# Optimization experiments

Hardware: AMD Instinct MI355X
Metric: run time of the kernel (lower is better)

The kernel has to match this reference:

```python
import jax, jax.numpy as jnp
import numpy as np

D_MODEL = 1024
D_STATE = 16
D_CONV = 4
EXPAND = 2
NUM_LAYERS = 2
SEQ = 1024
BATCH = 2
D_INNER = EXPAND * D_MODEL          # 2048
DT_RANK = (D_MODEL + 15) // 16      # 64 (math.ceil(d_model/16))


def setup_inputs() -> dict:
    key = jax.random.key(0)
    ks = jax.random.split(key, 10)
    s = 0.02
    # A initialized as in mamba_ssm: A = repeat(arange(1, d_state+1), d_inner) -> A_log = log(A)
    A_log = jnp.log(jnp.broadcast_to(
        jnp.arange(1, D_STATE + 1, dtype=jnp.float32), (NUM_LAYERS, D_INNER, D_STATE)))
    return {
        "pe": jax.random.normal(ks[0], (SEQ, D_MODEL), jnp.float32) * s,
        "condition": jax.random.normal(ks[1], (BATCH, SEQ, D_MODEL), jnp.float32),
        "W_in": jax.random.normal(ks[2], (NUM_LAYERS, 2 * D_INNER, D_MODEL), jnp.float32) * s,
        "conv_w": jax.random.normal(ks[3], (NUM_LAYERS, D_INNER, D_CONV), jnp.float32) * s,
        "conv_b": jnp.zeros((NUM_LAYERS, D_INNER), jnp.float32),
        "W_x": jax.random.normal(ks[4], (NUM_LAYERS, DT_RANK + 2 * D_STATE, D_INNER), jnp.float32) * s,
        "W_dt": jax.random.normal(ks[5], (NUM_LAYERS, D_INNER, DT_RANK), jnp.float32) * s,
        "b_dt": jax.random.normal(ks[6], (NUM_LAYERS, D_INNER), jnp.float32) * s,
        "A_log": A_log,
        "Dp": jnp.ones((NUM_LAYERS, D_INNER), jnp.float32),
        "W_out": jax.random.normal(ks[7], (NUM_LAYERS, D_MODEL, D_INNER), jnp.float32) * s,
        "output_shape": BATCH,
    }


def _mamba_block(x, W_in, conv_w, conv_b, W_x, W_dt, b_dt, A_log, Dp, W_out):
    # x: [B, L, d_model]
    B, L, _ = x.shape
    xz = jnp.einsum('bld,ed->ble', x, W_in)          # [B, L, 2*d_inner]
    u, z = jnp.split(xz, 2, axis=-1)                 # each [B, L, d_inner]
    # causal depthwise conv1d (padding=d_conv-1, truncate to L)
    xp = jnp.pad(u, ((0, 0), (D_CONV - 1, 0), (0, 0)))
    xc = conv_b + sum(conv_w[:, k] * xp[:, k:k + L, :] for k in range(D_CONV))
    xc = jax.nn.silu(xc)                             # [B, L, d_inner]
    x_dbl = jnp.einsum('bld,ed->ble', xc, W_x)       # [B, L, dt_rank + 2*d_state]
    dt, Bm, Cm = jnp.split(x_dbl, [DT_RANK, DT_RANK + D_STATE], axis=-1)
    delta = jax.nn.softplus(jnp.einsum('blr,dr->bld', dt, W_dt) + b_dt)  # [B, L, d_inner]
    A = -jnp.exp(A_log)                              # [d_inner, d_state]

    def step(h, inputs):
        u_t, d_t, B_t, C_t = inputs                  # [B,di],[B,di],[B,ds],[B,ds]
        dA = jnp.exp(d_t[:, :, None] * A)            # [B, di, ds]
        h = dA * h + (d_t * u_t)[:, :, None] * B_t[:, None, :]
        y = jnp.einsum('bds,bs->bd', h, C_t)
        return h, y

    h0 = jnp.zeros((B, D_INNER, D_STATE), x.dtype)
    xs = (xc.transpose(1, 0, 2), delta.transpose(1, 0, 2),
          Bm.transpose(1, 0, 2), Cm.transpose(1, 0, 2))
    _, ys = jax.lax.scan(step, h0, xs)               # ys: [L, B, d_inner]
    y = ys.transpose(1, 0, 2) + xc * Dp
    out = y * jax.nn.silu(z)
    return jnp.einsum('bld,ed->ble', out, W_out)     # [B, L, d_model]


def reference(pe, condition, W_in, conv_w, conv_b, W_x, W_dt, b_dt, A_log, Dp, W_out, output_shape):
    # pe.repeat(B,1,1) + condition
    x = pe[None, :, :] + condition
    for i in range(NUM_LAYERS):
        x = _mamba_block(x, W_in[i], conv_w[i], conv_b[i], W_x[i],
                         W_dt[i], b_dt[i], A_log[i], Dp[i], W_out[i])
    return x
```

## Files before the change

### kernel.cpp

```cpp
#include <hip/hip_runtime.h>
#include <math.h>

#define D_MODEL 1024
#define D_INNER 2048
#define D_STATE 16
#define DT_RANK 64
#define SEQ 1024
#define BATCH 2
#define NLAYERS 2
#define ROWS (BATCH*SEQ)
#define XDIM 96
#define XZLD (2*D_INNER)

#define NC 32
#define CL 32
#define SDB 256

#define G2_ROWS 64
#define G2_KC 128
#define G2_BK 32
#define G2_KS (D_INNER / G2_KC)

typedef short bf16x8 __attribute__((ext_vector_type(8)));
typedef float f32x4  __attribute__((ext_vector_type(4)));

__device__ __forceinline__ unsigned short f2bf(float f) {
    union { float f; unsigned int u; } v; v.f = f;
    unsigned int u = v.u;
    return (unsigned short)((u + 0x7FFFu + ((u >> 16) & 1u)) >> 16);
}
__device__ __forceinline__ float bf2f(unsigned short u) {
    union { unsigned int i; float f; } v; v.i = ((unsigned int)u) << 16; return v.f;
}

__device__ __forceinline__ void gload_lds16(const void* g, void* s) {
    __builtin_amdgcn_global_load_lds((const __attribute__((address_space(1))) void*)g,
                                     (__attribute__((address_space(3))) void*)s, 16, 0, 0);
}

__global__ __launch_bounds__(256) void add_pe_kernel(const float* __restrict__ pe,
    const float* __restrict__ cond, float* __restrict__ X)
{
    int i = blockIdx.x * 256 + threadIdx.x;
    int total = ROWS * D_MODEL / 4;
    if (i >= total) return;
    int row  = i / (D_MODEL / 4);
    int l    = row & (SEQ - 1);
    int col4 = i - row * (D_MODEL / 4);
    float4 p = reinterpret_cast<const float4*>(pe)[l * (D_MODEL / 4) + col4];
    float4 c = reinterpret_cast<const float4*>(cond)[i];
    float4 r; r.x = p.x + c.x; r.y = p.y + c.y; r.z = p.z + c.z; r.w = p.w + c.w;
    reinterpret_cast<float4*>(X)[i] = r;
}

__global__ __launch_bounds__(256) void conv_bf16_dense(const float* __restrict__ src,
    unsigned short* __restrict__ dst, int n4)
{
    int i = blockIdx.x * 256 + threadIdx.x;
    if (i >= n4) return;
    float4 v = reinterpret_cast<const float4*>(src)[i];
    ushort4 o; o.x = f2bf(v.x); o.y = f2bf(v.y); o.z = f2bf(v.z); o.w = f2bf(v.w);
    reinterpret_cast<ushort4*>(dst)[i] = o;
}

#define WN1 (NLAYERS * 2 * D_INNER * D_MODEL / 4)
#define WN2 (NLAYERS * D_MODEL * D_INNER / 4)
#define WN3 (NLAYERS * D_INNER * DT_RANK / 4)
#define WN4 (ROWS * D_MODEL / 4)
__global__ __launch_bounds__(256) void conv_wall(const float* __restrict__ Win,
    const float* __restrict__ Wout, const float* __restrict__ Wdt,
    const float* __restrict__ pe, const float* __restrict__ cond,
    unsigned short* __restrict__ WINbf, unsigned short* __restrict__ WOUTbf,
    unsigned short* __restrict__ WDTbf, unsigned short* __restrict__ Xbf)
{
    int i = blockIdx.x * 256 + threadIdx.x;
    if (i < WN1) {
        float4 v = reinterpret_cast<const float4*>(Win)[i];
        ushort4 o; o.x = f2bf(v.x); o.y = f2bf(v.y); o.z = f2bf(v.z); o.w = f2bf(v.w);
        reinterpret_cast<ushort4*>(WINbf)[i] = o;
    } else if (i < WN1 + WN2) {
        int j = i - WN1;
        float4 v = reinterpret_cast<const float4*>(Wout)[j];
        ushort4 o; o.x = f2bf(v.x); o.y = f2bf(v.y); o.z = f2bf(v.z); o.w = f2bf(v.w);
        reinterpret_cast<ushort4*>(WOUTbf)[j] = o;
    } else if (i < WN1 + WN2 + WN3) {
        int j = i - WN1 - WN2;
        float4 v = reinterpret_cast<const float4*>(Wdt)[j];
        ushort4 o; o.x = f2bf(v.x); o.y = f2bf(v.y); o.z = f2bf(v.z); o.w = f2bf(v.w);
        reinterpret_cast<ushort4*>(WDTbf)[j] = o;
    } else if (i < WN1 + WN2 + WN3 + WN4) {
        int j = i - WN1 - WN2 - WN3;
        int row  = j / (D_MODEL / 4);
        int l    = row & (SEQ - 1);
        int col4 = j - row * (D_MODEL / 4);
        float4 p = reinterpret_cast<const float4*>(pe)[l * (D_MODEL / 4) + col4];
        float4 c = reinterpret_cast<const float4*>(cond)[j];
        ushort4 o;
        o.x = f2bf(p.x + c.x); o.y = f2bf(p.y + c.y);
        o.z = f2bf(p.z + c.z); o.w = f2bf(p.w + c.w);
        reinterpret_cast<ushort4*>(Xbf)[j] = o;
    }
}

__global__ __launch_bounds__(256) void conv_bf16_strided(const float* __restrict__ src,
    int ld, int cols, unsigned short* __restrict__ dst, int total4)
{
    int i = blockIdx.x * 256 + threadIdx.x;
    if (i >= total4) return;
    int c4  = cols / 4;
    int row = i / c4;
    int col = (i - row * c4) * 4;
    float4 v = *reinterpret_cast<const float4*>(src + (size_t)row * ld + col);
    ushort4 o; o.x = f2bf(v.x); o.y = f2bf(v.y); o.z = f2bf(v.z); o.w = f2bf(v.w);
    *reinterpret_cast<ushort4*>(dst + (size_t)row * cols + col) = o;
}

__global__ __launch_bounds__(256) void conv_bf16_dtcols(const float* __restrict__ XDBL,
    unsigned short* __restrict__ dst)
{
    int i = blockIdx.x * 256 + threadIdx.x;
    if (i >= ROWS * DT_RANK / 4) return;
    int m  = i >> 4;
    int c4 = (i & 15) * 4;
    float4 v = *reinterpret_cast<const float4*>(XDBL + (size_t)m * XDIM + c4);
    ushort4 o; o.x = f2bf(v.x); o.y = f2bf(v.y); o.z = f2bf(v.z); o.w = f2bf(v.w);
    *reinterpret_cast<ushort4*>(dst + (size_t)m * DT_RANK + c4) = o;
}

#define GBM 128
#define GBN 128
#define GBK 64

#define GEMM_STAGE(Ap, Bp, lda, ldb, koff)                                      \
    _Pragma("unroll")                                                           \
    for (int i_ = 0; i_ < 4; ++i_) {                                            \
        int off_ = w * 4096 + i_ * 1024 + l * 16;                               \
        int row_ = off_ >> 7;                                                   \
        int col_ = (off_ & 127) >> 1;                                           \
        gload_lds16(Ap + (size_t)(m0 + row_) * (lda) + (koff) + col_,           \
                    (char*)As + w * 4096 + i_ * 1024);                          \
    }                                                                           \
    _Pragma("unroll")                                                           \
    for (int i_ = 0; i_ < 4; ++i_) {                                            \
        int off_ = w * 4096 + i_ * 1024 + l * 16;                               \
        int row_ = off_ >> 7;                                                   \
        int col_ = (off_ & 127) >> 1;                                           \
        gload_lds16(Bp + (size_t)(n0 + row_) * (ldb) + (koff) + col_,           \
                    (char*)Bs + w * 4096 + i_ * 1024);                          \
    }

#define GEMM_MFMA_STEP                                                          \
    _Pragma("unroll")                                                           \
    for (int kk = 0; kk < 2; ++kk) {                                            \
        bf16x8 af[4], bfr[4];                                                   \
        _Pragma("unroll")                                                       \
        for (int m = 0; m < 4; ++m)                                             \
            af[m] = *(const bf16x8*)&As[(wr * 64 + m * 16 + fr) * GBK + kk * 32 + fq * 8]; \
        _Pragma("unroll")                                                       \
        for (int n = 0; n < 4; ++n)                                             \
            bfr[n] = *(const bf16x8*)&Bs[(wc * 64 + n * 16 + fr) * GBK + kk * 32 + fq * 8]; \
        _Pragma("unroll")                                                       \
        for (int m = 0; m < 4; ++m)                                             \
            _Pragma("unroll")                                                   \
            for (int n = 0; n < 4; ++n)                                         \
                acc[m][n] = __builtin_amdgcn_mfma_f32_16x16x32_bf16(af[m], bfr[n], acc[m][n], 0, 0, 0); \
    }

__global__ __launch_bounds__(256) void gemm_bf16_nt(const unsigned short* __restrict__ A,
    const unsigned short* __restrict__ B, float* __restrict__ C,
    int M, int N, int K, int ldc, const float* __restrict__ bias, int epilogue)
{
    __shared__ unsigned short As[GBM * GBK];
    __shared__ unsigned short Bs[GBN * GBK];
    int tid = threadIdx.x;
    int w = tid >> 6, l = tid & 63;
    int wr = w >> 1, wc = w & 1;
    int m0 = blockIdx.y * GBM, n0 = blockIdx.x * GBN;

    f32x4 acc[4][4];
    #pragma unroll
    for (int m = 0; m < 4; ++m)
        #pragma unroll
        for (int n = 0; n < 4; ++n) acc[m][n] = (f32x4){0.f, 0.f, 0.f, 0.f};
    int fr = l & 15, fq = l >> 4;

    for (int k0 = 0; k0 < K; k0 += GBK) {
        GEMM_STAGE(A, B, K, K, k0)
        __syncthreads();
        GEMM_MFMA_STEP
        __syncthreads();
    }

    #pragma unroll
    for (int m = 0; m < 4; ++m)
        #pragma unroll
        for (int n = 0; n < 4; ++n) {
            int col = n0 + wc * 64 + n * 16 + fr;
            #pragma unroll
            for (int j = 0; j < 4; ++j) {
                int row = m0 + wr * 64 + m * 16 + fq * 4 + j;
                float v = acc[m][n][j];
                if (epilogue == 1) {
                    v += bias[col];
                    v = fmaxf(v, 0.f) + log1pf(__expf(-fabsf(v)));
                }
                C[(size_t)row * ldc + col] = v;
            }
        }
}

__global__ __launch_bounds__(256) void gemm_bf16_nt_bfout(const unsigned short* __restrict__ A,
    const unsigned short* __restrict__ B, unsigned short* __restrict__ C,
    int M, int N, int K, int ldc)
{
    __shared__ unsigned short As[GBM * GBK];
    __shared__ unsigned short Bs[GBN * GBK];
    int tid = threadIdx.x;
    int w = tid >> 6, l = tid & 63;
    int wr = w >> 1, wc = w & 1;
    int m0 = blockIdx.y * GBM, n0 = blockIdx.x * GBN;

    f32x4 acc[4][4];
    #pragma unroll
    for (int m = 0; m < 4; ++m)
        #pragma unroll
        for (int n = 0; n < 4; ++n) acc[m][n] = (f32x4){0.f, 0.f, 0.f, 0.f};
    int fr = l & 15, fq = l >> 4;

    for (int k0 = 0; k0 < K; k0 += GBK) {
        GEMM_STAGE(A, B, K, K, k0)
        __syncthreads();
        GEMM_MFMA_STEP
        __syncthreads();
    }

    #pragma unroll
    for (int m = 0; m < 4; ++m)
        #pragma unroll
        for (int n = 0; n < 4; ++n) {
            int col = n0 + wc * 64 + n * 16 + fr;
            #pragma unroll
            for (int j = 0; j < 4; ++j) {
                int row = m0 + wr * 64 + m * 16 + fq * 4 + j;
                C[(size_t)row * ldc + col] = f2bf(acc[m][n][j]);
            }
        }
}

__global__ __launch_bounds__(256) void gemm_bf16_sp_bfout(const unsigned short* __restrict__ A,
    const unsigned short* __restrict__ B, unsigned short* __restrict__ C,
    int M, int N, int K, int ldc, const float* __restrict__ bias)
{
    __shared__ unsigned short As[GBM * GBK];
    __shared__ unsigned short Bs[GBN * GBK];
    int tid = threadIdx.x;
    int w = tid >> 6, l = tid & 63;
    int wr = w >> 1, wc = w & 1;
    int m0 = blockIdx.y * GBM, n0 = blockIdx.x * GBN;

    f32x4 acc[4][4];
    #pragma unroll
    for (int m = 0; m < 4; ++m)
        #pragma unroll
        for (int n = 0; n < 4; ++n) acc[m][n] = (f32x4){0.f, 0.f, 0.f, 0.f};
    int fr = l & 15, fq = l >> 4;

    for (int k0 = 0; k0 < K; k0 += GBK) {
        GEMM_STAGE(A, B, K, K, k0)
        __syncthreads();
        GEMM_MFMA_STEP
        __syncthreads();
    }

    #pragma unroll
    for (int m = 0; m < 4; ++m)
        #pragma unroll
        for (int n = 0; n < 4; ++n) {
            int col = n0 + wc * 64 + n * 16 + fr;
            float bv = bias[col];
            #pragma unroll
            for (int j = 0; j < 4; ++j) {
                int row = m0 + wr * 64 + m * 16 + fq * 4 + j;
                float v = acc[m][n][j] + bv;
                v = fmaxf(v, 0.f) + log1pf(__expf(-fabsf(v)));
                C[(size_t)row * ldc + col] = f2bf(v);
            }
        }
}

__global__ __launch_bounds__(256) void gemm_bf16_nt_ks(const unsigned short* __restrict__ A, int lda,
    const unsigned short* __restrict__ B, int ldb, float* __restrict__ P,
    int M, int N, int Kper)
{
    __shared__ unsigned short As[GBM * GBK];
    __shared__ unsigned short Bs[GBN * GBK];
    int tid = threadIdx.x;
    int w = tid >> 6, l = tid & 63;
    int wr = w >> 1, wc = w & 1;
    int m0 = blockIdx.y * GBM, n0 = blockIdx.x * GBN;
    int koff = blockIdx.z * Kper;
    float* Pz = P + (size_t)blockIdx.z * M * N;

    f32x4 acc[4][4];
    #pragma unroll
    for (int m = 0; m < 4; ++m)
        #pragma unroll
        for (int n = 0; n < 4; ++n) acc[m][n] = (f32x4){0.f, 0.f, 0.f, 0.f};
    int fr = l & 15, fq = l >> 4;

    for (int k0 = 0; k0 < Kper; k0 += GBK) {
        GEMM_STAGE(A, B, lda, ldb, koff + k0)
        __syncthreads();
        GEMM_MFMA_STEP
        __syncthreads();
    }

    #pragma unroll
    for (int m = 0; m < 4; ++m)
        #pragma unroll
        for (int n = 0; n < 4; ++n) {
            int col = n0 + wc * 64 + n * 16 + fr;
            #pragma unroll
            for (int j = 0; j < 4; ++j) {
                int row = m0 + wr * 64 + m * 16 + fq * 4 + j;
                Pz[(size_t)row * N + col] = acc[m][n][j];
            }
        }
}

__global__ __launch_bounds__(256) void gemm4_reduce(const float* __restrict__ P,
    float* __restrict__ X, unsigned short* __restrict__ Xbf)
{
    int i = blockIdx.x * 256 + threadIdx.x;
    if (i >= ROWS * D_MODEL / 4) return;
    float4 a = reinterpret_cast<const float4*>(P)[i];
    float4 b = reinterpret_cast<const float4*>(P + (size_t)ROWS * D_MODEL)[i];
    float4 r; r.x = a.x + b.x; r.y = a.y + b.y; r.z = a.z + b.z; r.w = a.w + b.w;
    if (X) reinterpret_cast<float4*>(X)[i] = r;
    if (Xbf) {
        ushort4 o; o.x = f2bf(r.x); o.y = f2bf(r.y); o.z = f2bf(r.z); o.w = f2bf(r.w);
        reinterpret_cast<ushort4*>(Xbf)[i] = o;
    }
}

__global__ __launch_bounds__(256) void gemm2_fused(const unsigned short* __restrict__ XZbf,
    const float* __restrict__ cw, const float* __restrict__ cb,
    const float* __restrict__ B, float* __restrict__ P)
{
    __shared__ float Axc[G2_KC][68];
    __shared__ float Bs[G2_BK][XDIM + 1];
    int tid = threadIdx.x;
    int m0 = blockIdx.x * G2_ROWS;
    int kc = blockIdx.y;
    int k0 = kc * G2_KC;

    {
        int d_loc = tid & 127;
        int d     = k0 + d_loc;
        int r0    = m0 + (tid >> 7) * 32;
        float4 wv = *(const float4*)(cw + (size_t)d * 4);
        float cbv = cb[d];
        int l0 = r0 & (SEQ - 1);
        float u3 = (l0 >= 3) ? bf2f(XZbf[(size_t)(r0 - 3) * XZLD + d]) : 0.f;
        float u2 = (l0 >= 2) ? bf2f(XZbf[(size_t)(r0 - 2) * XZLD + d]) : 0.f;
        float u1 = (l0 >= 1) ? bf2f(XZbf[(size_t)(r0 - 1) * XZLD + d]) : 0.f;
        int rl0 = r0 - m0;
        #pragma unroll 4
        for (int t = 0; t < 32; ++t) {
            float u0 = bf2f(XZbf[(size_t)(r0 + t) * XZLD + d]);
            float v = cbv + wv.x * u3 + wv.y * u2 + wv.z * u1 + wv.w * u0;
            v = v / (1.f + __expf(-v));
            Axc[d_loc][rl0 + t] = v;
            u3 = u2; u2 = u1; u1 = u0;
        }
    }
    __syncthreads();

    int rg = tid >> 4;
    int cg = tid & 15;
    float acc[4][6];
    #pragma unroll
    for (int i = 0; i < 4; ++i)
        #pragma unroll
        for (int j = 0; j < 6; ++j) acc[i][j] = 0.f;

    for (int kb = 0; kb < G2_KC; kb += G2_BK) {
        {
            #pragma unroll
            for (int i = 0; i < 3; ++i) {
                int idx = tid + i * 256;
                int col = idx >> 3;
                int kk  = (idx & 7) * 4;
                float4 v = *(const float4*)(B + (size_t)col * D_INNER + k0 + kb + kk);
                Bs[kk + 0][col] = v.x;
                Bs[kk + 1][col] = v.y;
                Bs[kk + 2][col] = v.z;
                Bs[kk + 3][col] = v.w;
            }
        }
        __syncthreads();
        #pragma unroll
        for (int k = 0; k < G2_BK; ++k) {
            float4 a  = *(const float4*)&Axc[kb + k][rg * 4];
            float2 b0 = *(const float2*)&Bs[k][cg * 6];
            float2 b1 = *(const float2*)&Bs[k][cg * 6 + 2];
            float2 b2 = *(const float2*)&Bs[k][cg * 6 + 4];
            float av[4] = {a.x, a.y, a.z, a.w};
            float bv[6] = {b0.x, b0.y, b1.x, b1.y, b2.x, b2.y};
            #pragma unroll
            for (int i = 0; i < 4; ++i)
                #pragma unroll
                for (int j = 0; j < 6; ++j) acc[i][j] += av[i] * bv[j];
        }
        __syncthreads();
    }

    #pragma unroll
    for (int i = 0; i < 4; ++i)
        #pragma unroll
        for (int j = 0; j < 6; ++j)
            P[((size_t)kc * ROWS + m0 + rg * 4 + i) * XDIM + cg * 6 + j] = acc[i][j];
}

__global__ __launch_bounds__(256) void gemm2_splitk(const float* __restrict__ A,
    const float* __restrict__ B, float* __restrict__ P)
{
    __shared__ float As[G2_BK][G2_ROWS];
    __shared__ float Bs[G2_BK][XDIM + 1];
    int tid = threadIdx.x;
    int m0 = blockIdx.x * G2_ROWS;
    int kc = blockIdx.y;
    int k0 = kc * G2_KC;

    int rg = tid >> 4;
    int cg = tid & 15;
    float acc[4][6];
    #pragma unroll
    for (int i = 0; i < 4; ++i)
        #pragma unroll
        for (int j = 0; j < 6; ++j) acc[i][j] = 0.f;

    for (int kb = 0; kb < G2_KC; kb += G2_BK) {
        {
            int row = tid & 63;
            int kk  = (tid >> 6) * 4;
            #pragma unroll
            for (int i = 0; i < 2; ++i) {
                float4 v = *(const float4*)(A + (size_t)(m0 + row) * D_INNER + k0 + kb + kk + i * 16);
                As[kk + i * 16 + 0][row] = v.x;
                As[kk + i * 16 + 1][row] = v.y;
                As[kk + i * 16 + 2][row] = v.z;
                As[kk + i * 16 + 3][row] = v.w;
            }
        }
        {
            #pragma unroll
            for (int i = 0; i < 3; ++i) {
                int idx = tid + i * 256;
                int col = idx >> 3;
                int kk  = (idx & 7) * 4;
                float4 v = *(const float4*)(B + (size_t)col * D_INNER + k0 + kb + kk);
                Bs[kk + 0][col] = v.x;
                Bs[kk + 1][col] = v.y;
                Bs[kk + 2][col] = v.z;
                Bs[kk + 3][col] = v.w;
            }
        }
        __syncthreads();
        #pragma unroll
        for (int k = 0; k < G2_BK; ++k) {
            float4 a  = *(const float4*)&As[k][rg * 4];
            float2 b0 = *(const float2*)&Bs[k][cg * 6];
            float2 b1 = *(const float2*)&Bs[k][cg * 6 + 2];
            float2 b2 = *(const float2*)&Bs[k][cg * 6 + 4];
            float av[4] = {a.x, a.y, a.z, a.w};
            float bv[6] = {b0.x, b0.y, b1.x, b1.y, b2.x, b2.y};
            #pragma unroll
            for (int i = 0; i < 4; ++i)
                #pragma unroll
                for (int j = 0; j < 6; ++j) acc[i][j] += av[i] * bv[j];
        }
        __syncthreads();
    }

    #pragma unroll
    for (int i = 0; i < 4; ++i)
        #pragma unroll
        for (int j = 0; j < 6; ++j)
            P[((size_t)kc * ROWS + m0 + rg * 4 + i) * XDIM + cg * 6 + j] = acc[i][j];
}

__global__ __launch_bounds__(256) void gemm2_reduce(const float* __restrict__ P,
    float* __restrict__ XDBLo, unsigned short* __restrict__ dtbf)
{
    int i = blockIdx.x * 256 + threadIdx.x;
    if (i >= ROWS * XDIM / 4) return;
    float4 acc = make_float4(0.f, 0.f, 0.f, 0.f);
    #pragma unroll
    for (int ks = 0; ks < G2_KS; ++ks) {
        float4 v = *(const float4*)(P + (size_t)ks * ROWS * XDIM + (size_t)i * 4);
        acc.x += v.x; acc.y += v.y; acc.z += v.z; acc.w += v.w;
    }
    *(float4*)(XDBLo + (size_t)i * 4) = acc;
    if (dtbf) {
        int row = (i * 4) / XDIM;
        int col = (i * 4) - row * XDIM;
        if (col < DT_RANK) {
            ushort4 o; o.x = f2bf(acc.x); o.y = f2bf(acc.y); o.z = f2bf(acc.z); o.w = f2bf(acc.w);
            *reinterpret_cast<ushort4*>(dtbf + (size_t)row * DT_RANK + col) = o;
        }
    }
}

#define BM 64
#define BN 64
#define BK 16
__global__ __launch_bounds__(256) void gemm_nt(const float* __restrict__ A, int lda,
                                               const float* __restrict__ B, int ldb,
                                               float* __restrict__ C, int ldc,
                                               int M, int N, int K,
                                               const float* __restrict__ bias, int epilogue)
{
    __shared__ float As[BM][BK + 1];
    __shared__ float Bs[BN][BK + 1];
    int t  = threadIdx.x;
    int m0 = blockIdx.y * BM;
    int n0 = blockIdx.x * BN;
    int lrow = t >> 2;
    int lk   = (t & 3) * 4;
    int tm   = t >> 4;
    int tn   = t & 15;

    float acc[4][4];
    #pragma unroll
    for (int i = 0; i < 4; ++i)
        #pragma unroll
        for (int j = 0; j < 4; ++j) acc[i][j] = 0.f;

    for (int k0 = 0; k0 < K; k0 += BK) {
        {
            int row = m0 + lrow;
            float4 v = make_float4(0.f, 0.f, 0.f, 0.f);
            if (row < M) v = *reinterpret_cast<const float4*>(A + (size_t)row * lda + k0 + lk);
            As[lrow][lk + 0] = v.x; As[lrow][lk + 1] = v.y;
            As[lrow][lk + 2] = v.z; As[lrow][lk + 3] = v.w;
        }
        {
            int row = n0 + lrow;
            float4 v = make_float4(0.f, 0.f, 0.f, 0.f);
            if (row < N) v = *reinterpret_cast<const float4*>(B + (size_t)row * ldb + k0 + lk);
            Bs[lrow][lk + 0] = v.x; Bs[lrow][lk + 1] = v.y;
            Bs[lrow][lk + 2] = v.z; Bs[lrow][lk + 3] = v.w;
        }
        __syncthreads();
        #pragma unroll
        for (int kk = 0; kk < BK; ++kk) {
            float a[4], b[4];
            #pragma unroll
            for (int i = 0; i < 4; ++i) a[i] = As[tm * 4 + i][kk];
            #pragma unroll
            for (int j = 0; j < 4; ++j) b[j] = Bs[tn * 4 + j][kk];
            #pragma unroll
            for (int i = 0; i < 4; ++i)
                #pragma unroll
                for (int j = 0; j < 4; ++j) acc[i][j] += a[i] * b[j];
        }
        __syncthreads();
    }

    #pragma unroll
    for (int i = 0; i < 4; ++i) {
        int m = m0 + tm * 4 + i;
        if (m >= M) continue;
        #pragma unroll
        for (int j = 0; j < 4; ++j) {
            int n = n0 + tn * 4 + j;
            if (n >= N) continue;
            float v = acc[i][j];
            if (epilogue == 1) {
                v += bias[n];
                v = fmaxf(v, 0.f) + log1pf(__expf(-fabsf(v)));
            }
            C[(size_t)m * ldc + n] = v;
        }
    }
}

__global__ __launch_bounds__(256) void conv_silu_kernel(const float* __restrict__ XZ,
    const float* __restrict__ cw, const float* __restrict__ cb, float* __restrict__ XC)
{
    int idx = blockIdx.x * 256 + threadIdx.x;
    if (idx >= ROWS * (D_INNER / 4)) return;
    int d4   = idx % (D_INNER / 4);
    int rl   = idx / (D_INNER / 4);
    int l    = rl & (SEQ - 1);
    int base = rl - l;
    int d    = d4 * 4;

    float4 acc = reinterpret_cast<const float4*>(cb)[d4];
    float w[4][4];
    #pragma unroll
    for (int dd = 0; dd < 4; ++dd) {
        float4 wv = *reinterpret_cast<const float4*>(cw + (size_t)(d + dd) * 4);
        w[dd][0] = wv.x; w[dd][1] = wv.y; w[dd][2] = wv.z; w[dd][3] = wv.w;
    }
    #pragma unroll
    for (int k = 0; k < 4; ++k) {
        int lr = l - 3 + k;
        if (lr < 0) continue;
        float4 u = *reinterpret_cast<const float4*>(XZ + (size_t)(base + lr) * XZLD + d);
        acc.x += w[0][k] * u.x; acc.y += w[1][k] * u.y;
        acc.z += w[2][k] * u.z; acc.w += w[3][k] * u.w;
    }
    acc.x = acc.x / (1.f + __expf(-acc.x));
    acc.y = acc.y / (1.f + __expf(-acc.y));
    acc.z = acc.z / (1.f + __expf(-acc.z));
    acc.w = acc.w / (1.f + __expf(-acc.w));
    reinterpret_cast<float4*>(XC)[idx] = acc;
}


#define XC_ROLL_INIT                                                            \
    float4 wv = *(const float4*)(cw + (size_t)d * 4);                           \
    float cbv = cb[d];                                                          \
    float u3 = 0.f, u2 = 0.f, u1 = 0.f;                                         \
    if (c > 0) {                                                                \
        u3 = bf2f(XZbf[(r0 - 3) * XZLD + d]);                                   \
        u2 = bf2f(XZbf[(r0 - 2) * XZLD + d]);                                   \
        u1 = bf2f(XZbf[(r0 - 1) * XZLD + d]);                                   \
    }

#define XC_ROLL_STEP(uu_out)                                                    \
    float u0 = bf2f(XZbf[(r0 + t) * XZLD + d]);                                 \
    float cv_ = cbv + wv.x * u3 + wv.y * u2 + wv.z * u1 + wv.w * u0;            \
    float uu_out = cv_ / (1.f + __expf(-cv_));                                  \
    u3 = u2; u2 = u1; u1 = u0;

__global__ __launch_bounds__(SDB) void scan_part1c(const unsigned short* __restrict__ XZbf,
    const unsigned short* __restrict__ DL, const float* __restrict__ XDBL,
    const float* __restrict__ A_log, const float* __restrict__ cw,
    const float* __restrict__ cb, float* __restrict__ Psum, float* __restrict__ Ssum)
{
    __shared__ float sB[CL][16];
    int tid = threadIdx.x;
    int d = blockIdx.x * SDB + tid;
    int c = blockIdx.y, b = blockIdx.z;
    size_t r0 = (size_t)b * SEQ + (size_t)c * CL;

    if (tid < CL * 4) {
        int t = tid >> 2, j = (tid & 3) * 4;
        *(float4*)&sB[t][j] = *(const float4*)(XDBL + (r0 + t) * XDIM + DT_RANK + j);
    }

    float a[D_STATE], S[D_STATE];
    #pragma unroll
    for (int i = 0; i < 4; ++i) {
        float4 v = *(const float4*)(A_log + (size_t)d * D_STATE + i * 4);
        a[i*4+0] = -__expf(v.x); a[i*4+1] = -__expf(v.y);
        a[i*4+2] = -__expf(v.z); a[i*4+3] = -__expf(v.w);
    }
    #pragma unroll
    for (int s = 0; s < D_STATE; ++s) S[s] = 0.f;
    float sumdl = 0.f;
    XC_ROLL_INIT
    __syncthreads();

    for (int t = 0; t < CL; ++t) {
        float dl = bf2f(DL[(r0 + t) * D_INNER + d]);
        XC_ROLL_STEP(uu)
        float du = dl * uu;
        sumdl += dl;
        float4 b0 = *(const float4*)&sB[t][0];
        float4 b1 = *(const float4*)&sB[t][4];
        float4 b2 = *(const float4*)&sB[t][8];
        float4 b3 = *(const float4*)&sB[t][12];
        float bv[16] = {b0.x,b0.y,b0.z,b0.w, b1.x,b1.y,b1.z,b1.w,
                        b2.x,b2.y,b2.z,b2.w, b3.x,b3.y,b3.z,b3.w};
        #pragma unroll
        for (int s = 0; s < D_STATE; ++s) {
            float e = __expf(dl * a[s]);
            S[s] = e * S[s] + du * bv[s];
        }
    }

    size_t o = (((size_t)b * NC + c) * D_INNER + d) * D_STATE;
    #pragma unroll
    for (int i = 0; i < 4; ++i) {
        float4 p, s4;
        p.x = __expf(a[i*4+0] * sumdl); p.y = __expf(a[i*4+1] * sumdl);
        p.z = __expf(a[i*4+2] * sumdl); p.w = __expf(a[i*4+3] * sumdl);
        s4.x = S[i*4+0]; s4.y = S[i*4+1]; s4.z = S[i*4+2]; s4.w = S[i*4+3];
        *(float4*)(Psum + o + i * 4) = p;
        *(float4*)(Ssum + o + i * 4) = s4;
    }
}

__global__ __launch_bounds__(256) void scan_prefix(float* __restrict__ Psum,
    const float* __restrict__ Ssum)
{
    int idx = blockIdx.x * 256 + threadIdx.x;
    int b = idx >> 15;
    int rem = idx & 32767;
    float h = 0.f;
    for (int c = 0; c < NC; ++c) {
        size_t o = (((size_t)b * NC + c) * D_INNER * D_STATE) + rem;
        float p = Psum[o];
        float s = Ssum[o];
        Psum[o] = h;
        h = p * h + s;
    }
}

__global__ __launch_bounds__(SDB) void scan_part2c(const unsigned short* __restrict__ XZbf,
    unsigned short* __restrict__ DL, const float* __restrict__ XDBL,
    const float* __restrict__ A_log, const float* __restrict__ cw,
    const float* __restrict__ cb, const float* __restrict__ Dp,
    const float* __restrict__ Hin)
{
    __shared__ float sBC[CL][32];
    int tid = threadIdx.x;
    int d = blockIdx.x * SDB + tid;
    int c = blockIdx.y, b = blockIdx.z;
    size_t r0 = (size_t)b * SEQ + (size_t)c * CL;

    {
        int t = tid >> 3, j = (tid & 7) * 4;
        *(float4*)&sBC[t][j] = *(const float4*)(XDBL + (r0 + t) * XDIM + DT_RANK + j);
    }

    float a[D_STATE], h[D_STATE];
    #pragma unroll
    for (int i = 0; i < 4; ++i) {
        float4 v = *(const float4*)(A_log + (size_t)d * D_STATE + i * 4);
        a[i*4+0] = -__expf(v.x); a[i*4+1] = -__expf(v.y);
        a[i*4+2] = -__expf(v.z); a[i*4+3] = -__expf(v.w);
    }
    size_t ho = (((size_t)b * NC + c) * D_INNER + d) * D_STATE;
    #pragma unroll
    for (int i = 0; i < 4; ++i) {
        float4 v = *(const float4*)(Hin + ho + i * 4);
        h[i*4+0] = v.x; h[i*4+1] = v.y; h[i*4+2] = v.z; h[i*4+3] = v.w;
    }
    float dp = Dp[d];
    XC_ROLL_INIT
    __syncthreads();

    for (int t = 0; t < CL; ++t) {
        float dl = bf2f(DL[(r0 + t) * D_INNER + d]);
        float z  = bf2f(XZbf[(r0 + t) * XZLD + D_INNER + d]);
        XC_ROLL_STEP(uu)
        float du = dl * uu;
        float4 b0 = *(const float4*)&sBC[t][0];
        float4 b1 = *(const float4*)&sBC[t][4];
        float4 b2 = *(const float4*)&sBC[t][8];
        float4 b3 = *(const float4*)&sBC[t][12];
        float4 c0 = *(const float4*)&sBC[t][16];
        float4 c1 = *(const float4*)&sBC[t][20];
        float4 c2 = *(const float4*)&sBC[t][24];
        float4 c3 = *(const float4*)&sBC[t][28];
        float bv[16] = {b0.x,b0.y,b0.z,b0.w, b1.x,b1.y,b1.z,b1.w,
                        b2.x,b2.y,b2.z,b2.w, b3.x,b3.y,b3.z,b3.w};
        float cv[16] = {c0.x,c0.y,c0.z,c0.w, c1.x,c1.y,c1.z,c1.w,
                        c2.x,c2.y,c2.z,c2.w, c3.x,c3.y,c3.z,c3.w};
        float y = 0.f;
        #pragma unroll
        for (int s = 0; s < D_STATE; ++s) {
            float e = __expf(dl * a[s]);
            h[s] = e * h[s] + du * bv[s];
            y += h[s] * cv[s];
        }
        float sz = z / (1.f + __expf(-z));
        DL[(r0 + t) * D_INNER + d] = f2bf((y + uu * dp) * sz);
    }
}

__global__ __launch_bounds__(SDB) void scan_part1(const float* __restrict__ XC,
    const float* __restrict__ XZ, const float* __restrict__ XDBL,
    const float* __restrict__ A_log, float* __restrict__ Psum, float* __restrict__ Ssum)
{
    __shared__ float sB[CL][16];
    int tid = threadIdx.x;
    int d = blockIdx.x * SDB + tid;
    int c = blockIdx.y, b = blockIdx.z;
    size_t r0 = (size_t)b * SEQ + (size_t)c * CL;

    if (tid < CL * 4) {
        int t = tid >> 2, j = (tid & 3) * 4;
        *(float4*)&sB[t][j] = *(const float4*)(XDBL + (r0 + t) * XDIM + DT_RANK + j);
    }

    float a[D_STATE], S[D_STATE];
    #pragma unroll
    for (int i = 0; i < 4; ++i) {
        float4 v = *(const float4*)(A_log + (size_t)d * D_STATE + i * 4);
        a[i*4+0] = -__expf(v.x); a[i*4+1] = -__expf(v.y);
        a[i*4+2] = -__expf(v.z); a[i*4+3] = -__expf(v.w);
    }
    #pragma unroll
    for (int s = 0; s < D_STATE; ++s) S[s] = 0.f;
    float sumdl = 0.f;
    __syncthreads();

    for (int t = 0; t < CL; ++t) {
        float dl = XZ[(r0 + t) * XZLD + d];
        float uu = XC[(r0 + t) * D_INNER + d];
        float du = dl * uu;
        sumdl += dl;
        float4 b0 = *(const float4*)&sB[t][0];
        float4 b1 = *(const float4*)&sB[t][4];
        float4 b2 = *(const float4*)&sB[t][8];
        float4 b3 = *(const float4*)&sB[t][12];
        float bv[16] = {b0.x,b0.y,b0.z,b0.w, b1.x,b1.y,b1.z,b1.w,
                        b2.x,b2.y,b2.z,b2.w, b3.x,b3.y,b3.z,b3.w};
        #pragma unroll
        for (int s = 0; s < D_STATE; ++s) {
            float e = __expf(dl * a[s]);
            S[s] = e * S[s] + du * bv[s];
        }
    }

    size_t o = (((size_t)b * NC + c) * D_INNER + d) * D_STATE;
    #pragma unroll
    for (int i = 0; i < 4; ++i) {
        float4 p, s4;
        p.x = __expf(a[i*4+0] * sumdl); p.y = __expf(a[i*4+1] * sumdl);
        p.z = __expf(a[i*4+2] * sumdl); p.w = __expf(a[i*4+3] * sumdl);
        s4.x = S[i*4+0]; s4.y = S[i*4+1]; s4.z = S[i*4+2]; s4.w = S[i*4+3];
        *(float4*)(Psum + o + i * 4) = p;
        *(float4*)(Ssum + o + i * 4) = s4;
    }
}

__global__ __launch_bounds__(SDB) void scan_part2(const float* __restrict__ XC,
    float* __restrict__ XZ, const float* __restrict__ XDBL,
    const float* __restrict__ A_log, const float* __restrict__ Dp,
    const float* __restrict__ Hin)
{
    __shared__ float sBC[CL][32];
    int tid = threadIdx.x;
    int d = blockIdx.x * SDB + tid;
    int c = blockIdx.y, b = blockIdx.z;
    size_t r0 = (size_t)b * SEQ + (size_t)c * CL;

    {
        int t = tid >> 3, j = (tid & 7) * 4;
        *(float4*)&sBC[t][j] = *(const float4*)(XDBL + (r0 + t) * XDIM + DT_RANK + j);
    }

    float a[D_STATE], h[D_STATE];
    #pragma unroll
    for (int i = 0; i < 4; ++i) {
        float4 v = *(const float4*)(A_log + (size_t)d * D_STATE + i * 4);
        a[i*4+0] = -__expf(v.x); a[i*4+1] = -__expf(v.y);
        a[i*4+2] = -__expf(v.z); a[i*4+3] = -__expf(v.w);
    }
    size_t ho = (((size_t)b * NC + c) * D_INNER + d) * D_STATE;
    #pragma unroll
    for (int i = 0; i < 4; ++i) {
        float4 v = *(const float4*)(Hin + ho + i * 4);
        h[i*4+0] = v.x; h[i*4+1] = v.y; h[i*4+2] = v.z; h[i*4+3] = v.w;
    }
    float dp = Dp[d];
    __syncthreads();

    for (int t = 0; t < CL; ++t) {
        float dl = XZ[(r0 + t) * XZLD + d];
        float uu = XC[(r0 + t) * D_INNER + d];
        float z  = XZ[(r0 + t) * XZLD + D_INNER + d];
        float du = dl * uu;
        float4 b0 = *(const float4*)&sBC[t][0];
        float4 b1 = *(const float4*)&sBC[t][4];
        float4 b2 = *(const float4*)&sBC[t][8];
        float4 b3 = *(const float4*)&sBC[t][12];
        float4 c0 = *(const float4*)&sBC[t][16];
        float4 c1 = *(const float4*)&sBC[t][20];
        float4 c2 = *(const float4*)&sBC[t][24];
        float4 c3 = *(const float4*)&sBC[t][28];
        float bv[16] = {b0.x,b0.y,b0.z,b0.w, b1.x,b1.y,b1.z,b1.w,
                        b2.x,b2.y,b2.z,b2.w, b3.x,b3.y,b3.z,b3.w};
        float cv[16] = {c0.x,c0.y,c0.z,c0.w, c1.x,c1.y,c1.z,c1.w,
                        c2.x,c2.y,c2.z,c2.w, c3.x,c3.y,c3.z,c3.w};
        float y = 0.f;
        #pragma unroll
        for (int s = 0; s < D_STATE; ++s) {
            float e = __expf(dl * a[s]);
            h[s] = e * h[s] + du * bv[s];
            y += h[s] * cv[s];
        }
        float sz = z / (1.f + __expf(-z));
        XZ[(r0 + t) * XZLD + d] = (y + uu * dp) * sz;
    }
}

__global__ __launch_bounds__(256) void scan_kernel2(const float* __restrict__ XC,
    float* __restrict__ XZ, const float* __restrict__ XDBL,
    const float* __restrict__ A_log, const float* __restrict__ Dp)
{
    int tid = threadIdx.x;
    int s  = tid & 15;
    int dd = tid >> 4;
    int d  = blockIdx.x * 16 + dd;
    int b  = blockIdx.y;

    float a  = -__expf(A_log[(size_t)d * D_STATE + s]);
    float h  = 0.f;
    float dp = Dp[d];
    const size_t rbase = (size_t)b * SEQ;

    for (int t = 0; t < SEQ; ++t) {
        size_t r = rbase + t;
        float dl = XZ[r * XZLD + d];
        float uu = XC[r * D_INNER + d];
        float z  = XZ[r * XZLD + D_INNER + d];
        float Bv = XDBL[r * XDIM + DT_RANK + s];
        float Cv = XDBL[r * XDIM + DT_RANK + D_STATE + s];
        float e  = __expf(dl * a);
        h = e * h + dl * uu * Bv;
        float y = h * Cv;
        y += __shfl_xor(y, 1);
        y += __shfl_xor(y, 2);
        y += __shfl_xor(y, 4);
        y += __shfl_xor(y, 8);
        if (s == 0) {
            float sz = z / (1.f + __expf(-z));
            XZ[r * XZLD + d] = (y + uu * dp) * sz;
        }
    }
}

extern "C" void kernel_launch(void* const* d_in, const int* in_sizes, int n_in,
                              void* d_out, int out_size, void* d_ws, size_t ws_size,
                              hipStream_t stream)
{
    const float* pe    = (const float*)d_in[0];
    const float* cond  = (const float*)d_in[1];
    const float* W_in  = (const float*)d_in[2];
    const float* cw    = (const float*)d_in[3];
    const float* cb    = (const float*)d_in[4];
    const float* W_x   = (const float*)d_in[5];
    const float* W_dt  = (const float*)d_in[6];
    const float* b_dt  = (const float*)d_in[7];
    const float* A_log = (const float*)d_in[8];
    const float* Dp    = (const float*)d_in[9];
    const float* W_out = (const float*)d_in[10];

    float* X = (float*)d_out;

    char* wsp = (char*)d_ws;
    unsigned short* XZbf = (unsigned short*)wsp;
    float* XDBL  = (float*)(wsp + 33554432);
    unsigned short* BF0   = (unsigned short*)(wsp + 34340864);
    unsigned short* dtbf  = (unsigned short*)(wsp + 42729472);
    unsigned short* WINbf = (unsigned short*)(wsp + 42991616);
    unsigned short* WOUTbf= (unsigned short*)(wsp + 59768832);
    unsigned short* WDTbf = (unsigned short*)(wsp + 68157440);
    float* SCR   = (float*)(wsp + 68681728);
    size_t need_A = 68681728 + 16777216;

    float* XZb   = (float*)d_ws;
    float* XCb   = XZb + (size_t)ROWS * XZLD;
    float* XDBLb = XCb + (size_t)ROWS * D_INNER;
    void* rest = (void*)(XDBLb + (size_t)ROWS * XDIM);
    unsigned short* Abf = (unsigned short*)rest;
    unsigned short* Bbf = Abf + (size_t)ROWS * D_INNER;
    float* PpartB = (float*)rest;
    float* PsumB  = (float*)rest;
    float* SsumB  = PsumB + (size_t)BATCH * NC * D_INNER * D_STATE;
    size_t need_B = ((size_t)ROWS * XZLD + (size_t)ROWS * D_INNER + (size_t)ROWS * XDIM) * 4
                  + ((size_t)ROWS * D_INNER + (size_t)ROWS * D_INNER) * 2;

    if (ws_size >= need_A) {
        float* Psum = SCR;
        float* Ssum = SCR + (size_t)BATCH * NC * D_INNER * D_STATE;

        conv_wall<<<(WN1 + WN2 + WN3 + WN4 + 255) / 256, 256, 0, stream>>>(
            W_in, W_out, W_dt, pe, cond, WINbf, WOUTbf, WDTbf, BF0);

        for (int l = 0; l < NLAYERS; ++l) {
            const unsigned short* WINl  = WINbf  + (size_t)l * 2 * D_INNER * D_MODEL;
            const unsigned short* WOUTl = WOUTbf + (size_t)l * D_MODEL * D_INNER;
            const unsigned short* WDTl  = WDTbf  + (size_t)l * D_INNER * DT_RANK;
            const float* W_x_l   = W_x   + (size_t)l * XDIM * D_INNER;
            const float* cw_l    = cw    + (size_t)l * D_INNER * 4;
            const float* cb_l    = cb    + (size_t)l * D_INNER;
            const float* b_dt_l  = b_dt  + (size_t)l * D_INNER;
            const float* A_log_l = A_log + (size_t)l * D_INNER * D_STATE;
            const float* Dp_l    = Dp    + (size_t)l * D_INNER;

            gemm_bf16_nt_bfout<<<dim3(2 * D_INNER / GBN, ROWS / GBM), 256, 0, stream>>>(
                BF0, WINl, XZbf, ROWS, 2 * D_INNER, D_MODEL, XZLD);
            gemm2_fused<<<dim3(ROWS / G2_ROWS, G2_KS), 256, 0, stream>>>(
                XZbf, cw_l, cb_l, W_x_l, SCR);
            gemm2_reduce<<<(ROWS * XDIM / 4 + 255) / 256, 256, 0, stream>>>(SCR, XDBL, dtbf);
            gemm_bf16_sp_bfout<<<dim3(D_INNER / GBN, ROWS / GBM), 256, 0, stream>>>(
                dtbf, WDTl, BF0, ROWS, D_INNER, DT_RANK, D_INNER, b_dt_l);
            scan_part1c<<<dim3(D_INNER / SDB, NC, BATCH), SDB, 0, stream>>>(
                XZbf, BF0, XDBL, A_log_l, cw_l, cb_l, Psum, Ssum);
            scan_prefix<<<BATCH * D_INNER * D_STATE / 256, 256, 0, stream>>>(Psum, Ssum);
            scan_part2c<<<dim3(D_INNER / SDB, NC, BATCH), SDB, 0, stream>>>(
                XZbf, BF0, XDBL, A_log_l, cw_l, cb_l, Dp_l, Psum);
            gemm_bf16_nt_ks<<<dim3(D_MODEL / GBN, ROWS / GBM, 2), 256, 0, stream>>>(
                BF0, D_INNER, WOUTl, D_INNER, SCR, ROWS, D_MODEL, D_INNER / 2);
            gemm4_reduce<<<(ROWS * D_MODEL / 4 + 255) / 256, 256, 0, stream>>>(
                SCR, (l == NLAYERS - 1) ? X : nullptr, (l < NLAYERS - 1) ? BF0 : nullptr);
        }
    } else if (ws_size >= need_B) {
        add_pe_kernel<<<ROWS * D_MODEL / 4 / 256, 256, 0, stream>>>(pe, cond, X);
        for (int l = 0; l < NLAYERS; ++l) {
            const float* W_in_l  = W_in  + (size_t)l * 2 * D_INNER * D_MODEL;
            const float* W_out_l = W_out + (size_t)l * D_MODEL * D_INNER;
            const float* W_x_l   = W_x   + (size_t)l * XDIM * D_INNER;
            const float* W_dt_l  = W_dt  + (size_t)l * D_INNER * DT_RANK;
            const float* b_dt_l  = b_dt  + (size_t)l * D_INNER;
            const float* A_log_l = A_log + (size_t)l * D_INNER * D_STATE;
            const float* Dp_l    = Dp    + (size_t)l * D_INNER;

            conv_bf16_dense<<<(ROWS * D_MODEL / 4 + 255) / 256, 256, 0, stream>>>(X, Abf, ROWS * D_MODEL / 4);
            conv_bf16_dense<<<(2 * D_INNER * D_MODEL / 4 + 255) / 256, 256, 0, stream>>>(W_in_l, Bbf, 2 * D_INNER * D_MODEL / 4);
            gemm_bf16_nt<<<dim3(2 * D_INNER / GBN, ROWS / GBM), 256, 0, stream>>>(
                Abf, Bbf, XZb, ROWS, 2 * D_INNER, D_MODEL, XZLD, nullptr, 0);
            conv_silu_kernel<<<ROWS * (D_INNER / 4) / 256, 256, 0, stream>>>(
                XZb, cw + (size_t)l * D_INNER * 4, cb + (size_t)l * D_INNER, XCb);
            gemm2_splitk<<<dim3(ROWS / G2_ROWS, G2_KS), 256, 0, stream>>>(XCb, W_x_l, PpartB);
            gemm2_reduce<<<(ROWS * XDIM / 4 + 255) / 256, 256, 0, stream>>>(PpartB, XDBLb, nullptr);
            conv_bf16_dtcols<<<(ROWS * DT_RANK / 4 + 255) / 256, 256, 0, stream>>>(XDBLb, Abf);
            conv_bf16_dense<<<(D_INNER * DT_RANK / 4 + 255) / 256, 256, 0, stream>>>(W_dt_l, Bbf, D_INNER * DT_RANK / 4);
            gemm_bf16_nt<<<dim3(D_INNER / GBN, ROWS / GBM), 256, 0, stream>>>(
                Abf, Bbf, XZb, ROWS, D_INNER, DT_RANK, XZLD, b_dt_l, 1);
            scan_part1<<<dim3(D_INNER / SDB, NC, BATCH), SDB, 0, stream>>>(
                XCb, XZb, XDBLb, A_log_l, PsumB, SsumB);
            scan_prefix<<<BATCH * D_INNER * D_STATE / 256, 256, 0, stream>>>(PsumB, SsumB);
            scan_part2<<<dim3(D_INNER / SDB, NC, BATCH), SDB, 0, stream>>>(
                XCb, XZb, XDBLb, A_log_l, Dp_l, PsumB);
            conv_bf16_strided<<<(ROWS * D_INNER / 4 + 255) / 256, 256, 0, stream>>>(
                XZb, XZLD, D_INNER, Abf, ROWS * D_INNER / 4);
            conv_bf16_dense<<<(D_MODEL * D_INNER / 4 + 255) / 256, 256, 0, stream>>>(W_out_l, Bbf, D_MODEL * D_INNER / 4);
            gemm_bf16_nt<<<dim3(D_MODEL / GBN, ROWS / GBM), 256, 0, stream>>>(
                Abf, Bbf, X, ROWS, D_MODEL, D_INNER, D_MODEL, nullptr, 0);
        }
    } else {
        add_pe_kernel<<<ROWS * D_MODEL / 4 / 256, 256, 0, stream>>>(pe, cond, X);
        for (int l = 0; l < NLAYERS; ++l) {
            gemm_nt<<<dim3(2 * D_INNER / BN, ROWS / BM), 256, 0, stream>>>(
                X, D_MODEL, W_in + (size_t)l * 2 * D_INNER * D_MODEL, D_MODEL,
                XZb, XZLD, ROWS, 2 * D_INNER, D_MODEL, nullptr, 0);
            conv_silu_kernel<<<ROWS * (D_INNER / 4) / 256, 256, 0, stream>>>(
                XZb, cw + (size_t)l * D_INNER * 4, cb + (size_t)l * D_INNER, XCb);
            gemm_nt<<<dim3((XDIM + BN - 1) / BN, ROWS / BM), 256, 0, stream>>>(
                XCb, D_INNER, W_x + (size_t)l * XDIM * D_INNER, D_INNER,
                XDBLb, XDIM, ROWS, XDIM, D_INNER, nullptr, 0);
            gemm_nt<<<dim3(D_INNER / BN, ROWS / BM), 256, 0, stream>>>(
                XDBLb, XDIM, W_dt + (size_t)l * D_INNER * DT_RANK, DT_RANK,
                XZb, XZLD, ROWS, D_INNER, DT_RANK, b_dt + (size_t)l * D_INNER, 1);
            scan_kernel2<<<dim3(D_INNER / 16, BATCH), 256, 0, stream>>>(
                XCb, XZb, XDBLb, A_log + (size_t)l * D_INNER * D_STATE, Dp + (size_t)l * D_INNER);
            gemm_nt<<<dim3(D_MODEL / BN, ROWS / BM), 256, 0, stream>>>(
                XZb, XZLD, W_out + (size_t)l * D_MODEL * D_INNER, D_INNER,
                X, D_MODEL, ROWS, D_MODEL, D_INNER, nullptr, 0);
        }
    }
}
```

Baseline: 362.6 us.

## Replace per-state exp with power tree and materialize conv output in bf16

```diff
diff --git a/kernel.cpp b/kernel.cpp
--- a/kernel.cpp
+++ b/kernel.cpp
@@ -37,6 +37,12 @@
     __builtin_amdgcn_global_load_lds((const __attribute__((address_space(1))) void*)g,
                                      (__attribute__((address_space(3))) void*)s, 16, 0, 0);
 }
+
+#define POW_TREE(E, e1)                                                         \
+    E[0] = e1;          E[1] = e1 * e1;   E[2] = E[1] * e1;  E[3] = E[1] * E[1];\
+    E[4] = E[3] * E[0]; E[5] = E[3] * E[1]; E[6] = E[3] * E[2]; E[7] = E[3] * E[3];\
+    E[8] = E[7] * E[0]; E[9] = E[7] * E[1]; E[10] = E[7] * E[2]; E[11] = E[7] * E[3];\
+    E[12] = E[7] * E[4]; E[13] = E[7] * E[5]; E[14] = E[7] * E[6]; E[15] = E[7] * E[7];
 
 __global__ __launch_bounds__(256) void add_pe_kernel(const float* __restrict__ pe,
     const float* __restrict__ cond, float* __restrict__ X)
@@ -345,7 +351,8 @@
 
 __global__ __launch_bounds__(256) void gemm2_fused(const unsigned short* __restrict__ XZbf,
     const float* __restrict__ cw, const float* __restrict__ cb,
-    const float* __restrict__ B, float* __restrict__ P)
+    const float* __restrict__ B, unsigned short* __restrict__ XCbf,
+    float* __restrict__ P)
 {
     __shared__ float Axc[G2_KC][68];
     __shared__ float Bs[G2_BK][XDIM + 1];
@@ -371,6 +378,7 @@
             float v = cbv + wv.x * u3 + wv.y * u2 + wv.z * u1 + wv.w * u0;
             v = v / (1.f + __expf(-v));
             Axc[d_loc][rl0 + t] = v;
+            XCbf[(size_t)(r0 + t) * D_INNER + d] = f2bf(v);
             u3 = u2; u2 = u1; u1 = u0;
         }
     }
@@ -620,26 +628,9 @@
 }
 
 
-#define XC_ROLL_INIT                                                            \
-    float4 wv = *(const float4*)(cw + (size_t)d * 4);                           \
-    float cbv = cb[d];                                                          \
-    float u3 = 0.f, u2 = 0.f, u1 = 0.f;                                         \
-    if (c > 0) {                                                                \
-        u3 = bf2f(XZbf[(r0 - 3) * XZLD + d]);                                   \
-        u2 = bf2f(XZbf[(r0 - 2) * XZLD + d]);                                   \
-        u1 = bf2f(XZbf[(r0 - 1) * XZLD + d]);                                   \
-    }
-
-#define XC_ROLL_STEP(uu_out)                                                    \
-    float u0 = bf2f(XZbf[(r0 + t) * XZLD + d]);                                 \
-    float cv_ = cbv + wv.x * u3 + wv.y * u2 + wv.z * u1 + wv.w * u0;            \
-    float uu_out = cv_ / (1.f + __expf(-cv_));                                  \
-    u3 = u2; u2 = u1; u1 = u0;
-
-__global__ __launch_bounds__(SDB) void scan_part1c(const unsigned short* __restrict__ XZbf,
+__global__ __launch_bounds__(SDB) void scan_part1b(const unsigned short* __restrict__ XCbf,
     const unsigned short* __restrict__ DL, const float* __restrict__ XDBL,
-    const float* __restrict__ A_log, const float* __restrict__ cw,
-    const float* __restrict__ cb, float* __restrict__ Psum, float* __restrict__ Ssum)
+    const float* __restrict__ A_log, float* __restrict__ Psum, float* __restrict__ Ssum)
 {
     __shared__ float sB[CL][16];
     int tid = threadIdx.x;
@@ -659,27 +650,51 @@
         a[i*4+0] = -__expf(v.x); a[i*4+1] = -__expf(v.y);
         a[i*4+2] = -__expf(v.z); a[i*4+3] = -__expf(v.w);
     }
+    bool powok = true;
+    #pragma unroll
+    for (int s = 0; s < D_STATE; ++s)
+        powok = powok && (fabsf(a[s] + (float)(s + 1)) < 1e-3f * (float)(s + 1));
     #pragma unroll
     for (int s = 0; s < D_STATE; ++s) S[s] = 0.f;
     float sumdl = 0.f;
-    XC_ROLL_INIT
     __syncthreads();
 
-    for (int t = 0; t < CL; ++t) {
-        float dl = bf2f(DL[(r0 + t) * D_INNER + d]);
-        XC_ROLL_STEP(uu)
-        float du = dl * uu;
-        sumdl += dl;
-        float4 b0 = *(const float4*)&sB[t][0];
-        float4 b1 = *(const float4*)&sB[t][4];
-        float4 b2 = *(const float4*)&sB[t][8];
-        float4 b3 = *(const float4*)&sB[t][12];
-        float bv[16] = {b0.x,b0.y,b0.z,b0.w, b1.x,b1.y,b1.z,b1.w,
-                        b2.x,b2.y,b2.z,b2.w, b3.x,b3.y,b3.z,b3.w};
-        #pragma unroll
-        for (int s = 0; s < D_STATE; ++s) {
-            float e = __expf(dl * a[s]);
-            S[s] = e * S[s] + du * bv[s];
+    if (powok) {
+        for (int t = 0; t < CL; ++t) {
+            float dl = bf2f(DL[(r0 + t) * D_INNER + d]);
+            float uu = bf2f(XCbf[(r0 + t) * D_INNER + d]);
+            float du = dl * uu;
+            sumdl += dl;
+            float4 b0 = *(const float4*)&sB[t][0];
+            float4 b1 = *(const float4*)&sB[t][4];
+            float4 b2 = *(const float4*)&sB[t][8];
+            float4 b3 = *(const float4*)&sB[t][12];
+            float bv[16] = {b0.x,b0.y,b0.z,b0.w, b1.x,b1.y,b1.z,b1.w,
+                            b2.x,b2.y,b2.z,b2.w, b3.x,b3.y,b3.z,b3.w};
+            float e1 = __expf(-dl);
+            float E[16];
+            POW_TREE(E, e1)
+            #pragma unroll
+            for (int s = 0; s < D_STATE; ++s)
+                S[s] = E[s] * S[s] + du * bv[s];
+        }
+    } else {
+        for (int t = 0; t < CL; ++t) {
+            float dl = bf2f(DL[(r0 + t) * D_INNER + d]);
+            float uu = bf2f(XCbf[(r0 + t) * D_INNER + d]);
+            float du = dl * uu;
+            sumdl += dl;
+            float4 b0 = *(const float4*)&sB[t][0];
+            float4 b1 = *(const float4*)&sB[t][4];
+            float4 b2 = *(const float4*)&sB[t][8];
+            float4 b3 = *(const float4*)&sB[t][12];
+            float bv[16] = {b0.x,b0.y,b0.z,b0.w, b1.x,b1.y,b1.z,b1.w,
+                            b2.x,b2.y,b2.z,b2.w, b3.x,b3.y,b3.z,b3.w};
+            #pragma unroll
+            for (int s = 0; s < D_STATE; ++s) {
+                float e = __expf(dl * a[s]);
+                S[s] = e * S[s] + du * bv[s];
+            }
         }
     }
 
@@ -711,11 +726,10 @@
     }
 }
 
-__global__ __launch_bounds__(SDB) void scan_part2c(const unsigned short* __restrict__ XZbf,
-    unsigned short* __restrict__ DL, const float* __restrict__ XDBL,
-    const float* __restrict__ A_log, const float* __restrict__ cw,
-    const float* __restrict__ cb, const float* __restrict__ Dp,
-    const float* __restrict__ Hin)
+__global__ __launch_bounds__(SDB) void scan_part2b(const unsigned short* __restrict__ XCbf,
+    unsigned short* __restrict__ DL, const unsigned short* __restrict__ XZbf,
+    const float* __restrict__ XDBL, const float* __restrict__ A_log,
+    const float* __restrict__ Dp, const float* __restrict__ Hin)
 {
     __shared__ float sBC[CL][32];
     int tid = threadIdx.x;
@@ -735,6 +749,10 @@
         a[i*4+0] = -__expf(v.x); a[i*4+1] = -__expf(v.y);
         a[i*4+2] = -__expf(v.z); a[i*4+3] = -__expf(v.w);
     }
+    bool powok = true;
+    #pragma unroll
+    for (int s = 0; s < D_STATE; ++s)
+        powok = powok && (fabsf(a[s] + (float)(s + 1)) < 1e-3f * (float)(s + 1));
     size_t ho = (((size_t)b * NC + c) * D_INNER + d) * D_STATE;
     #pragma unroll
     for (int i = 0; i < 4; ++i) {
@@ -742,35 +760,66 @@
         h[i*4+0] = v.x; h[i*4+1] = v.y; h[i*4+2] = v.z; h[i*4+3] = v.w;
     }
     float dp = Dp[d];
-    XC_ROLL_INIT
     __syncthreads();
 
-    for (int t = 0; t < CL; ++t) {
-        float dl = bf2f(DL[(r0 + t) * D_INNER + d]);
-        float z  = bf2f(XZbf[(r0 + t) * XZLD + D_INNER + d]);
-        XC_ROLL_STEP(uu)
-        float du = dl * uu;
-        float4 b0 = *(const float4*)&sBC[t][0];
-        float4 b1 = *(const float4*)&sBC[t][4];
-        float4 b2 = *(const float4*)&sBC[t][8];
-        float4 b3 = *(const float4*)&sBC[t][12];
-        float4 c0 = *(const float4*)&sBC[t][16];
-        float4 c1 = *(const float4*)&sBC[t][20];
-        float4 c2 = *(const float4*)&sBC[t][24];
-        float4 c3 = *(const float4*)&sBC[t][28];
-        float bv[16] = {b0.x,b0.y,b0.z,b0.w, b1.x,b1.y,b1.z,b1.w,
-                        b2.x,b2.y,b2.z,b2.w, b3.x,b3.y,b3.z,b3.w};
-        float cv[16] = {c0.x,c0.y,c0.z,c0.w, c1.x,c1.y,c1.z,c1.w,
-                        c2.x,c2.y,c2.z,c2.w, c3.x,c3.y,c3.z,c3.w};
-        float y = 0.f;
-        #pragma unroll
-        for (int s = 0; s < D_STATE; ++s) {
-            float e = __expf(dl * a[s]);
-            h[s] = e * h[s] + du * bv[s];
-            y += h[s] * cv[s];
-        }
-        float sz = z / (1.f + __expf(-z));
-        DL[(r0 + t) * D_INNER + d] = f2bf((y + uu * dp) * sz);
+    if (powok) {
+        for (int t = 0; t < CL; ++t) {
+            float dl = bf2f(DL[(r0 + t) * D_INNER + d]);
+            float uu = bf2f(XCbf[(r0 + t) * D_INNER + d]);
+            float z  = bf2f(XZbf[(r0 + t) * XZLD + D_INNER + d]);
+            float du = dl * uu;
+            float4 b0 = *(const float4*)&sBC[t][0];
+            float4 b1 = *(const float4*)&sBC[t][4];
+            float4 b2 = *(const float4*)&sBC[t][8];
+            float4 b3 = *(const float4*)&sBC[t][12];
+            float4 c0 = *(const float4*)&sBC[t][16];
+            float4 c1 = *(const float4*)&sBC[t][20];
+            float4 c2 = *(const float4*)&sBC[t][24];
+            float4 c3 = *(const float4*)&sBC[t][28];
+            float bv[16] = {b0.x,b0.y,b0.z,b0.w, b1.x,b1.y,b1.z,b1.w,
+                            b2.x,b2.y,b2.z,b2.w, b3.x,b3.y,b3.z,b3.w};
+            float cv[16] = {c0.x,c0.y,c0.z,c0.w, c1.x,c1.y,c1.z,c1.w,
+                            c2.x,c2.y,c2.z,c2.w, c3.x,c3.y,c3.z,c3.w};
+            float e1 = __expf(-dl);
+            float E[16];
+            POW_TREE(E, e1)
+            float y = 0.f;
+            #pragma unroll
+            for (int s = 0; s < D_STATE; ++s) {
+                h[s] = E[s] * h[s] + du * bv[s];
+                y += h[s] * cv[s];
+            }
+            float sz = z / (1.f + __expf(-z));
+            DL[(r0 + t) * D_INNER + d] = f2bf((y + uu * dp) * sz);
+        }
+    } else {
+        for (int t = 0; t < CL; ++t) {
+            float dl = bf2f(DL[(r0 + t) * D_INNER + d]);
+            float uu = bf2f(XCbf[(r0 + t) * D_INNER + d]);
+            float z  = bf2f(XZbf[(r0 + t) * XZLD + D_INNER + d]);
+            float du = dl * uu;
+            float4 b0 = *(const float4*)&sBC[t][0];
+            float4 b1 = *(const float4*)&sBC[t][4];
+            float4 b2 = *(const float4*)&sBC[t][8];
+            float4 b3 = *(const float4*)&sBC[t][12];
+            float4 c0 = *(const float4*)&sBC[t][16];
+            float4 c1 = *(const float4*)&sBC[t][20];
+            float4 c2 = *(const float4*)&sBC[t][24];
+            float4 c3 = *(const float4*)&sBC[t][28];
+            float bv[16] = {b0.x,b0.y,b0.z,b0.w, b1.x,b1.y,b1.z,b1.w,
+                            b2.x,b2.y,b2.z,b2.w, b3.x,b3.y,b3.z,b3.w};
+            float cv[16] = {c0.x,c0.y,c0.z,c0.w, c1.x,c1.y,c1.z,c1.w,
+                            c2.x,c2.y,c2.z,c2.w, c3.x,c3.y,c3.z,c3.w};
+            float y = 0.f;
+            #pragma unroll
+            for (int s = 0; s < D_STATE; ++s) {
+                float e = __expf(dl * a[s]);
+                h[s] = e * h[s] + du * bv[s];
+                y += h[s] * cv[s];
+            }
+            float sz = z / (1.f + __expf(-z));
+            DL[(r0 + t) * D_INNER + d] = f2bf((y + uu * dp) * sz);
+        }
     }
 }
 
@@ -948,6 +997,7 @@
 
     char* wsp = (char*)d_ws;
     unsigned short* XZbf = (unsigned short*)wsp;
+    unsigned short* XCbf = (unsigned short*)(wsp + 16777216);
     float* XDBL  = (float*)(wsp + 33554432);
     unsigned short* BF0   = (unsigned short*)(wsp + 34340864);
     unsigned short* dtbf  = (unsigned short*)(wsp + 42729472);
@@ -990,15 +1040,15 @@
             gemm_bf16_nt_bfout<<<dim3(2 * D_INNER / GBN, ROWS / GBM), 256, 0, stream>>>(
                 BF0, WINl, XZbf, ROWS, 2 * D_INNER, D_MODEL, XZLD);
             gemm2_fused<<<dim3(ROWS / G2_ROWS, G2_KS), 256, 0, stream>>>(
-                XZbf, cw_l, cb_l, W_x_l, SCR);
+                XZbf, cw_l, cb_l, W_x_l, XCbf, SCR);
             gemm2_reduce<<<(ROWS * XDIM / 4 + 255) / 256, 256, 0, stream>>>(SCR, XDBL, dtbf);
             gemm_bf16_sp_bfout<<<dim3(D_INNER / GBN, ROWS / GBM), 256, 0, stream>>>(
                 dtbf, WDTl, BF0, ROWS, D_INNER, DT_RANK, D_INNER, b_dt_l);
-            scan_part1c<<<dim3(D_INNER / SDB, NC, BATCH), SDB, 0, stream>>>(
-                XZbf, BF0, XDBL, A_log_l, cw_l, cb_l, Psum, Ssum);
+            scan_part1b<<<dim3(D_INNER / SDB, NC, BATCH), SDB, 0, stream>>>(
+                XCbf, BF0, XDBL, A_log_l, Psum, Ssum);
             scan_prefix<<<BATCH * D_INNER * D_STATE / 256, 256, 0, stream>>>(Psum, Ssum);
-            scan_part2c<<<dim3(D_INNER / SDB, NC, BATCH), SDB, 0, stream>>>(
-                XZbf, BF0, XDBL, A_log_l, cw_l, cb_l, Dp_l, Psum);
+            scan_part2b<<<dim3(D_INNER / SDB, NC, BATCH), SDB, 0, stream>>>(
+                XCbf, BF0, XZbf, XDBL, A_log_l, Dp_l, Psum);
             gemm_bf16_nt_ks<<<dim3(D_MODEL / GBN, ROWS / GBM, 2), 256, 0, stream>>>(
                 BF0, D_INNER, WOUTl, D_INNER, SCR, ROWS, D_MODEL, D_INNER / 2);
             gemm4_reduce<<<(ROWS * D_MODEL / 4 + 255) / 256, 256, 0, stream>>>(
```

After: 321.3 us (median of 2 runs). 1.13x faster.
